# Performance work log

Hardware: AMD Instinct MI355X
Metric: run time of the kernel (lower is better)

## Reference

```python
import jax, jax.numpy as jnp
import numpy as np

N_NODES = 100000
IN_DIM = 256
HIDDEN = 512
N_INC = 1000000   # incidence (gather/scatter) list length
N_SEG = 100000    # number of hyperedges / segments


def setup_inputs() -> dict:
    key = jax.random.key(0)
    ks = jax.random.split(key, 6)
    x = jax.random.normal(ks[0], (N_NODES, IN_DIM), dtype=jnp.float32)
    target_nodes = jax.random.randint(ks[1], (N_INC,), 0, N_NODES, dtype=jnp.int32)
    target_ids = jnp.sort(jax.random.randint(ks[2], (N_INC,), 0, N_SEG, dtype=jnp.int32))
    # Linear params (PyTorch stores [out,in]; we keep [in,out] and matmul directly)
    W1 = jax.random.normal(ks[3], (IN_DIM, HIDDEN), dtype=jnp.float32) * (1.0 / np.sqrt(IN_DIM))
    b1 = jnp.zeros((HIDDEN,), dtype=jnp.float32)
    W2 = jax.random.normal(ks[4], (HIDDEN, 1), dtype=jnp.float32) * (1.0 / np.sqrt(HIDDEN))
    b2 = jnp.zeros((1,), dtype=jnp.float32)
    return {"x": x, "target_nodes": target_nodes, "target_ids": target_ids,
            "num_segments": N_SEG, "W1": W1, "b1": b1, "W2": W2, "b2": b2}


def reference(x, target_nodes, target_ids, num_segments, W1, b1, W2, b2):
    # gather node features, scatter-sum into segments (hyperedges)
    gathered = x[target_nodes, :]                                   # [N_INC, IN_DIM]
    Z = jax.ops.segment_sum(gathered, target_ids,
                            num_segments=num_segments)              # [N_SEG, IN_DIM]
    Z = jnp.maximum(Z @ W1 + b1, 0.0)                               # linear + relu
    # dropout is identity in eval mode
    Z = Z @ W2 + b2                                                 # [N_SEG, 1]
    return jax.nn.sigmoid(Z)[:, 0]                                  # squeeze(-1)
```

## Files before the change

### kernel.cpp

```cpp
#include <hip/hip_runtime.h>
#include <hip/hip_bf16.h>
#include <math.h>

#define N_NODES   100000
#define IN_DIM    256
#define HIDDEN    512
#define N_INC     1000000
#define N_SEG     100000

typedef __attribute__((ext_vector_type(8))) short bf16x8;
typedef __attribute__((ext_vector_type(4))) float f32x4;

__device__ __forceinline__ unsigned short f2bf(float f) {
  unsigned int u = __builtin_bit_cast(unsigned int, f);
  u += 0x7FFFu + ((u >> 16) & 1u);
  return (unsigned short)(u >> 16);
}
__device__ __forceinline__ float bflo(unsigned int u) {
  return __builtin_bit_cast(float, u << 16);
}
__device__ __forceinline__ float bfhi(unsigned int u) {
  return __builtin_bit_cast(float, u & 0xFFFF0000u);
}
__device__ __forceinline__ unsigned pack2(float a, float b) {
  return (unsigned)f2bf(a) | ((unsigned)f2bf(b) << 16);
}

__global__ void k_seg_starts(const int* __restrict__ ids, int* __restrict__ starts) {
  int s = blockIdx.x * blockDim.x + threadIdx.x;
  if (s > N_SEG) return;
  int lo = 0, hi = N_INC;
  while (lo < hi) {
    int mid = (lo + hi) >> 1;
    if (ids[mid] < s) lo = mid + 1; else hi = mid;
  }
  starts[s] = lo;
}

__global__ void k_w1t(const float* __restrict__ W1, unsigned short* __restrict__ W1t) {
  int idx = blockIdx.x * 256 + threadIdx.x;
  int k  = idx >> 7;
  int c4 = idx & 127;
  float4 v = *(const float4*)(W1 + (size_t)k * HIDDEN + c4 * 4);
  W1t[(c4 * 4 + 0) * IN_DIM + k] = f2bf(v.x);
  W1t[(c4 * 4 + 1) * IN_DIM + k] = f2bf(v.y);
  W1t[(c4 * 4 + 2) * IN_DIM + k] = f2bf(v.z);
  W1t[(c4 * 4 + 3) * IN_DIM + k] = f2bf(v.w);
}

__global__ void k_xbf(const float* __restrict__ x, unsigned short* __restrict__ xb) {
  size_t idx = (size_t)blockIdx.x * 256 + threadIdx.x;
  float4 v = *(const float4*)(x + idx * 4);
  uint2 p;
  p.x = pack2(v.x, v.y);
  p.y = pack2(v.z, v.w);
  *(uint2*)(xb + idx * 4) = p;
}

#define ACC8(v)                                                        \
  acc0 += bflo((v).x); acc1 += bfhi((v).x);                            \
  acc2 += bflo((v).y); acc3 += bfhi((v).y);                            \
  acc4 += bflo((v).z); acc5 += bfhi((v).z);                            \
  acc6 += bflo((v).w); acc7 += bfhi((v).w);

__global__ void k_segsum(const unsigned short* __restrict__ xb, const int* __restrict__ nodes,
                         const int* __restrict__ starts, unsigned short* __restrict__ Zb) {
  int wave = threadIdx.x >> 6;
  int lane = threadIdx.x & 63;
  int s = blockIdx.x * 4 + wave;
  if (s >= N_SEG) return;
  const int beg = starts[s];
  const int end = starts[s + 1];
  const int half = lane >> 5;
  const int sl   = lane & 31;
  const unsigned short* base = xb + sl * 8;
  float acc0 = 0.f, acc1 = 0.f, acc2 = 0.f, acc3 = 0.f;
  float acc4 = 0.f, acc5 = 0.f, acc6 = 0.f, acc7 = 0.f;
  int j = beg + half;
  for (; j + 6 < end; j += 8) {
    int n0 = nodes[j], n1 = nodes[j + 2], n2 = nodes[j + 4], n3 = nodes[j + 6];
    uint4 v0 = *(const uint4*)(base + (size_t)n0 * IN_DIM);
    uint4 v1 = *(const uint4*)(base + (size_t)n1 * IN_DIM);
    uint4 v2 = *(const uint4*)(base + (size_t)n2 * IN_DIM);
    uint4 v3 = *(const uint4*)(base + (size_t)n3 * IN_DIM);
    ACC8(v0); ACC8(v1); ACC8(v2); ACC8(v3);
  }
  for (; j < end; j += 2) {
    int n0 = nodes[j];
    uint4 v0 = *(const uint4*)(base + (size_t)n0 * IN_DIM);
    ACC8(v0);
  }
  acc0 += __shfl_xor(acc0, 32, 64);
  acc1 += __shfl_xor(acc1, 32, 64);
  acc2 += __shfl_xor(acc2, 32, 64);
  acc3 += __shfl_xor(acc3, 32, 64);
  acc4 += __shfl_xor(acc4, 32, 64);
  acc5 += __shfl_xor(acc5, 32, 64);
  acc6 += __shfl_xor(acc6, 32, 64);
  acc7 += __shfl_xor(acc7, 32, 64);
  if (half == 0) {
    uint4 p;
    p.x = pack2(acc0, acc1);
    p.y = pack2(acc2, acc3);
    p.z = pack2(acc4, acc5);
    p.w = pack2(acc6, acc7);
    *(uint4*)(Zb + (size_t)s * IN_DIM + sl * 8) = p;
  }
}

__global__ __launch_bounds__(256, 2) void k_mlp(
    const unsigned short* __restrict__ Zb, const unsigned short* __restrict__ W1t,
    const float* __restrict__ b1, const float* __restrict__ W2,
    const float* __restrict__ b2, float* __restrict__ out) {
  __shared__ __align__(16) unsigned short Bf[2][8][64][8];
  const int tid  = threadIdx.x;
  const int wave = tid >> 6;
  const int lane = tid & 63;
  const int m0   = blockIdx.x * 128 + wave * 32;

  uint4 a[2][8];
  const int arow = m0 + (lane & 15);
  const int ak   = (lane >> 4) * 8;
  #pragma unroll
  for (int kc = 0; kc < 8; ++kc) {
    #pragma unroll
    for (int rf = 0; rf < 2; ++rf) {
      int row = arow + rf * 16;
      if (row < N_NODES)
        a[rf][kc] = *(const uint4*)(Zb + (size_t)row * IN_DIM + kc * 32 + ak);
      else
        a[rf][kc] = make_uint4(0u, 0u, 0u, 0u);
    }
  }

  float logit[2][4];
  #pragma unroll
  for (int rf = 0; rf < 2; ++rf)
    #pragma unroll
    for (int e = 0; e < 4; ++e) logit[rf][e] = 0.f;

  for (int nt = 0; nt < 4; ++nt) {
    const int c0 = nt * 128;
    f32x4 acc[2][8];
    #pragma unroll
    for (int rf = 0; rf < 2; ++rf)
      #pragma unroll
      for (int cf = 0; cf < 8; ++cf) acc[rf][cf] = (f32x4){0.f, 0.f, 0.f, 0.f};

    for (int ks = 0; ks < 4; ++ks) {
      #pragma unroll
      for (int it = 0; it < 4; ++it) {
        int idx  = it * 256 + tid;
        int sub  = idx >> 9;
        int rem  = idx & 511;
        int frag = rem >> 6;
        int l2   = rem & 63;
        int col  = c0 + frag * 16 + (l2 & 15);
        int kk   = (ks * 2 + sub) * 32 + (l2 >> 4) * 8;
        *(uint4*)&Bf[sub][frag][l2][0] = *(const uint4*)(W1t + col * IN_DIM + kk);
      }
      __syncthreads();
      #pragma unroll
      for (int sub = 0; sub < 2; ++sub) {
        int kc = ks * 2 + sub;
        bf16x8 av0 = __builtin_bit_cast(bf16x8, a[0][kc]);
        bf16x8 av1 = __builtin_bit_cast(bf16x8, a[1][kc]);
        #pragma unroll
        for (int cf = 0; cf < 8; ++cf) {
          bf16x8 bv = *(const bf16x8*)&Bf[sub][cf][lane][0];
          acc[0][cf] = __builtin_amdgcn_mfma_f32_16x16x32_bf16(av0, bv, acc[0][cf], 0, 0, 0);
          acc[1][cf] = __builtin_amdgcn_mfma_f32_16x16x32_bf16(av1, bv, acc[1][cf], 0, 0, 0);
        }
      }
      __syncthreads();
    }
    #pragma unroll
    for (int cf = 0; cf < 8; ++cf) {
      int c = c0 + cf * 16 + (lane & 15);
      float bb = b1[c];
      float w2 = W2[c];
      #pragma unroll
      for (int rf = 0; rf < 2; ++rf)
        #pragma unroll
        for (int e = 0; e < 4; ++e) {
          float h = acc[rf][cf][e] + bb;
          h = h > 0.f ? h : 0.f;
          logit[rf][e] = fmaf(h, w2, logit[rf][e]);
        }
    }
  }
  #pragma unroll
  for (int rf = 0; rf < 2; ++rf)
    #pragma unroll
    for (int e = 0; e < 4; ++e) {
      float v = logit[rf][e];
      v += __shfl_xor(v, 1, 64);
      v += __shfl_xor(v, 2, 64);
      v += __shfl_xor(v, 4, 64);
      v += __shfl_xor(v, 8, 64);
      logit[rf][e] = v;
    }
  if ((lane & 15) == 0) {
    float bb2 = b2[0];
    #pragma unroll
    for (int rf = 0; rf < 2; ++rf)
      #pragma unroll
      for (int e = 0; e < 4; ++e) {
        int row = m0 + rf * 16 + (lane >> 4) * 4 + e;
        if (row < N_NODES)
          out[row] = 1.f / (1.f + expf(-(logit[rf][e] + bb2)));
      }
  }
}

extern "C" void kernel_launch(void* const* d_in, const int* in_sizes, int n_in,
                              void* d_out, int out_size, void* d_ws, size_t ws_size,
                              hipStream_t stream) {
  const float* x   = (const float*)d_in[0];
  const int* nodes = (const int*)d_in[1];
  const int* ids   = (const int*)d_in[2];
  const float* W1  = (const float*)d_in[4];
  const float* b1  = (const float*)d_in[5];
  const float* W2  = (const float*)d_in[6];
  const float* b2  = (const float*)d_in[7];
  float* out       = (float*)d_out;

  char* ws = (char*)d_ws;
  int* starts = (int*)ws;
  size_t off = (((size_t)(N_SEG + 1) * sizeof(int)) + 1023) & ~(size_t)1023;
  unsigned short* Zb = (unsigned short*)(ws + off);
  off += (size_t)N_NODES * IN_DIM * sizeof(unsigned short);
  off = (off + 1023) & ~(size_t)1023;
  unsigned short* W1t = (unsigned short*)(ws + off);
  off += (size_t)HIDDEN * IN_DIM * sizeof(unsigned short);
  off = (off + 1023) & ~(size_t)1023;
  unsigned short* xb = (unsigned short*)(ws + off);

  k_seg_starts<<<(N_SEG + 1 + 255) / 256, 256, 0, stream>>>(ids, starts);
  k_w1t<<<128, 256, 0, stream>>>(W1, W1t);
  k_xbf<<<(N_NODES * IN_DIM / 4) / 256 + 1, 256, 0, stream>>>(x, xb);
  k_segsum<<<(N_SEG + 3) / 4, 256, 0, stream>>>(xb, nodes, starts, Zb);
  k_mlp<<<(N_NODES + 127) / 128, 256, 0, stream>>>(Zb, W1t, b1, W2, b2, out);
}
```

Measured before the change: 164.2 us.

## Fuse segment-sum gather into MLP kernel via swizzled LDS tile

Merges the segment-sum and MLP kernels: each block gathers and sums 128 segments into a swizzled shared-memory tile, then runs the bf16 MFMA MLP directly from it. This removes the global write and reread of the intermediate Z matrix and one kernel launch. In exchange each block uses about 80KB of LDS and each wave processes 32 segments serially, which sharply reduces the parallelism available to hide gather latency.

```diff
diff --git a/kernel.cpp b/kernel.cpp
--- a/kernel.cpp
+++ b/kernel.cpp
@@ -63,73 +63,69 @@
   acc4 += bflo((v).z); acc5 += bfhi((v).z);                            \
   acc6 += bflo((v).w); acc7 += bfhi((v).w);
 
-__global__ void k_segsum(const unsigned short* __restrict__ xb, const int* __restrict__ nodes,
-                         const int* __restrict__ starts, unsigned short* __restrict__ Zb) {
-  int wave = threadIdx.x >> 6;
-  int lane = threadIdx.x & 63;
-  int s = blockIdx.x * 4 + wave;
-  if (s >= N_SEG) return;
-  const int beg = starts[s];
-  const int end = starts[s + 1];
-  const int half = lane >> 5;
-  const int sl   = lane & 31;
-  const unsigned short* base = xb + sl * 8;
-  float acc0 = 0.f, acc1 = 0.f, acc2 = 0.f, acc3 = 0.f;
-  float acc4 = 0.f, acc5 = 0.f, acc6 = 0.f, acc7 = 0.f;
-  int j = beg + half;
-  for (; j + 6 < end; j += 8) {
-    int n0 = nodes[j], n1 = nodes[j + 2], n2 = nodes[j + 4], n3 = nodes[j + 6];
-    uint4 v0 = *(const uint4*)(base + (size_t)n0 * IN_DIM);
-    uint4 v1 = *(const uint4*)(base + (size_t)n1 * IN_DIM);
-    uint4 v2 = *(const uint4*)(base + (size_t)n2 * IN_DIM);
-    uint4 v3 = *(const uint4*)(base + (size_t)n3 * IN_DIM);
-    ACC8(v0); ACC8(v1); ACC8(v2); ACC8(v3);
-  }
-  for (; j < end; j += 2) {
-    int n0 = nodes[j];
-    uint4 v0 = *(const uint4*)(base + (size_t)n0 * IN_DIM);
-    ACC8(v0);
-  }
-  acc0 += __shfl_xor(acc0, 32, 64);
-  acc1 += __shfl_xor(acc1, 32, 64);
-  acc2 += __shfl_xor(acc2, 32, 64);
-  acc3 += __shfl_xor(acc3, 32, 64);
-  acc4 += __shfl_xor(acc4, 32, 64);
-  acc5 += __shfl_xor(acc5, 32, 64);
-  acc6 += __shfl_xor(acc6, 32, 64);
-  acc7 += __shfl_xor(acc7, 32, 64);
-  if (half == 0) {
-    uint4 p;
-    p.x = pack2(acc0, acc1);
-    p.y = pack2(acc2, acc3);
-    p.z = pack2(acc4, acc5);
-    p.w = pack2(acc6, acc7);
-    *(uint4*)(Zb + (size_t)s * IN_DIM + sl * 8) = p;
-  }
-}
-
-__global__ __launch_bounds__(256, 2) void k_mlp(
-    const unsigned short* __restrict__ Zb, const unsigned short* __restrict__ W1t,
+__global__ __launch_bounds__(256, 2) void k_fused(
+    const unsigned short* __restrict__ xb, const int* __restrict__ nodes,
+    const int* __restrict__ starts, const unsigned short* __restrict__ W1t,
     const float* __restrict__ b1, const float* __restrict__ W2,
     const float* __restrict__ b2, float* __restrict__ out) {
+  __shared__ __align__(16) unsigned short Zt[128 * 256];
   __shared__ __align__(16) unsigned short Bf[2][8][64][8];
   const int tid  = threadIdx.x;
   const int wave = tid >> 6;
   const int lane = tid & 63;
-  const int m0   = blockIdx.x * 128 + wave * 32;
+  const int m0   = blockIdx.x * 128;
+  const int half = lane >> 5;
+  const int sl   = lane & 31;
+  const unsigned short* gbase = xb + sl * 8;
+
+  for (int t = 0; t < 32; ++t) {
+    const int s_local = wave * 32 + t;
+    const int s = m0 + s_local;
+    int beg = 0, end = 0;
+    if (s < N_SEG) { beg = starts[s]; end = starts[s + 1]; }
+    float acc0 = 0.f, acc1 = 0.f, acc2 = 0.f, acc3 = 0.f;
+    float acc4 = 0.f, acc5 = 0.f, acc6 = 0.f, acc7 = 0.f;
+    int j = beg + half;
+    for (; j + 6 < end; j += 8) {
+      int n0 = nodes[j], n1 = nodes[j + 2], n2 = nodes[j + 4], n3 = nodes[j + 6];
+      uint4 v0 = *(const uint4*)(gbase + (size_t)n0 * IN_DIM);
+      uint4 v1 = *(const uint4*)(gbase + (size_t)n1 * IN_DIM);
+      uint4 v2 = *(const uint4*)(gbase + (size_t)n2 * IN_DIM);
+      uint4 v3 = *(const uint4*)(gbase + (size_t)n3 * IN_DIM);
+      ACC8(v0); ACC8(v1); ACC8(v2); ACC8(v3);
+    }
+    for (; j < end; j += 2) {
+      int n0 = nodes[j];
+      uint4 v0 = *(const uint4*)(gbase + (size_t)n0 * IN_DIM);
+      ACC8(v0);
+    }
+    acc0 += __shfl_xor(acc0, 32, 64);
+    acc1 += __shfl_xor(acc1, 32, 64);
+    acc2 += __shfl_xor(acc2, 32, 64);
+    acc3 += __shfl_xor(acc3, 32, 64);
+    acc4 += __shfl_xor(acc4, 32, 64);
+    acc5 += __shfl_xor(acc5, 32, 64);
+    acc6 += __shfl_xor(acc6, 32, 64);
+    acc7 += __shfl_xor(acc7, 32, 64);
+    if (half == 0) {
+      uint4 p;
+      p.x = pack2(acc0, acc1);
+      p.y = pack2(acc2, acc3);
+      p.z = pack2(acc4, acc5);
+      p.w = pack2(acc6, acc7);
+      int off = (s_local * 256 + sl * 8) ^ ((s_local & 7) << 3);
+      *(uint4*)&Zt[off] = p;
+    }
+  }
 
   uint4 a[2][8];
-  const int arow = m0 + (lane & 15);
-  const int ak   = (lane >> 4) * 8;
   #pragma unroll
   for (int kc = 0; kc < 8; ++kc) {
     #pragma unroll
     for (int rf = 0; rf < 2; ++rf) {
-      int row = arow + rf * 16;
-      if (row < N_NODES)
-        a[rf][kc] = *(const uint4*)(Zb + (size_t)row * IN_DIM + kc * 32 + ak);
-      else
-        a[rf][kc] = make_uint4(0u, 0u, 0u, 0u);
+      int r_local = wave * 32 + rf * 16 + (lane & 15);
+      int off = (r_local * 256 + kc * 32 + (lane >> 4) * 8) ^ ((r_local & 7) << 3);
+      a[rf][kc] = *(const uint4*)&Zt[off];
     }
   }
 
@@ -206,7 +202,7 @@
     for (int rf = 0; rf < 2; ++rf)
       #pragma unroll
       for (int e = 0; e < 4; ++e) {
-        int row = m0 + rf * 16 + (lane >> 4) * 4 + e;
+        int row = m0 + wave * 32 + rf * 16 + (lane >> 4) * 4 + e;
         if (row < N_NODES)
           out[row] = 1.f / (1.f + expf(-(logit[rf][e] + bb2)));
       }
@@ -228,9 +224,6 @@
   char* ws = (char*)d_ws;
   int* starts = (int*)ws;
   size_t off = (((size_t)(N_SEG + 1) * sizeof(int)) + 1023) & ~(size_t)1023;
-  unsigned short* Zb = (unsigned short*)(ws + off);
-  off += (size_t)N_NODES * IN_DIM * sizeof(unsigned short);
-  off = (off + 1023) & ~(size_t)1023;
   unsigned short* W1t = (unsigned short*)(ws + off);
   off += (size_t)HIDDEN * IN_DIM * sizeof(unsigned short);
   off = (off + 1023) & ~(size_t)1023;
@@ -239,6 +232,5 @@
   k_seg_starts<<<(N_SEG + 1 + 255) / 256, 256, 0, stream>>>(ids, starts);
   k_w1t<<<128, 256, 0, stream>>>(W1, W1t);
   k_xbf<<<(N_NODES * IN_DIM / 4) / 256 + 1, 256, 0, stream>>>(x, xb);
-  k_segsum<<<(N_SEG + 3) / 4, 256, 0, stream>>>(xb, nodes, starts, Zb);
-  k_mlp<<<(N_NODES + 127) / 128, 256, 0, stream>>>(Zb, W1t, b1, W2, b2, out);
-}
+  k_fused<<<(N_SEG + 127) / 128, 256, 0, stream>>>(xb, nodes, starts, W1t, b1, W2, b2, out);
+}
```

Result: slower. 232.4 us (+41.5%).
